# Kernel tuning notes

Hardware: AMD Instinct MI355X
Metric: run time of the kernel (lower is better)

The kernel has to match this reference:

```python
import jax, jax.numpy as jnp
import numpy as np

N, D, H = 262144, 512, 128


def _mlp(x, W1, b1, W2, b2):
    # Linear -> ReLU -> Linear
    return jax.nn.relu(x @ W1 + b1) @ W2 + b2


def setup_inputs() -> dict:
    key = jax.random.key(0)
    ks = jax.random.split(key, 8)
    features = jax.random.normal(ks[0], (N, D), dtype=jnp.float32)
    # last column is the routing flag: 0 -> transform expert, nonzero -> actor expert
    flags = jax.random.randint(ks[1], (N,), 0, 2).astype(jnp.float32)
    features = features.at[:, -1].set(flags)
    s = 0.02
    return {
        "features": features,
        "Wt1": jax.random.normal(ks[2], (D, H), dtype=jnp.float32) * s,
        "bt1": jnp.zeros((H,), dtype=jnp.float32),
        "Wt2": jax.random.normal(ks[3], (H, H), dtype=jnp.float32) * s,
        "bt2": jnp.zeros((H,), dtype=jnp.float32),
        "Wa1": jax.random.normal(ks[4], (D, H), dtype=jnp.float32) * s,
        "ba1": jnp.zeros((H,), dtype=jnp.float32),
        "Wa2": jax.random.normal(ks[5], (H, H), dtype=jnp.float32) * s,
        "ba2": jnp.zeros((H,), dtype=jnp.float32),
        "Wv1": jax.random.normal(ks[6], (D, H), dtype=jnp.float32) * s,
        "bv1": jnp.zeros((H,), dtype=jnp.float32),
        "Wv2": jax.random.normal(ks[7], (H, H), dtype=jnp.float32) * s,
        "bv2": jnp.zeros((H,), dtype=jnp.float32),
    }


def reference(features, Wt1, bt1, Wt2, bt2, Wa1, ba1, Wa2, ba2, Wv1, bv1, Wv2, bv2):
    # forward_actor: per-row dispatch on flag = features[:, -1]
    # flag == 0 -> policy_transform_net, else -> policy_actor_net.
    # Equivalent vectorized form: compute both experts, select per row.
    flag_is_zero = (features[:, -1] == 0)[:, None]  # [N, 1]
    trans_out = _mlp(features, Wt1, bt1, Wt2, bt2)   # [N, H]
    actor_out = _mlp(features, Wa1, ba1, Wa2, ba2)   # [N, H]
    latent_pi = jnp.where(flag_is_zero, trans_out, actor_out)
    # forward_critic: Linear-ReLU-Linear-ReLU
    latent_vf = jax.nn.relu(_mlp(features, Wv1, bv1, Wv2, bv2))
    return latent_pi, latent_vf
```

## Files before the change

### kernel.cpp

```cpp
#include <hip/hip_runtime.h>

#define NTOK 262144L
#define DIN 512
#define HID 128

typedef __attribute__((ext_vector_type(4))) float f32x4;
typedef __attribute__((ext_vector_type(8))) short bf16x8;

static __device__ __forceinline__ unsigned short f2bf(float f) {
  unsigned int u = __builtin_bit_cast(unsigned int, f);
  u += 0x7fffu + ((u >> 16) & 1u);
  return (unsigned short)(u >> 16);
}

__global__ void pack_w(const float* __restrict__ Wt1, const float* __restrict__ Wa1,
                       const float* __restrict__ Wv1, const float* __restrict__ Wt2,
                       const float* __restrict__ Wa2, const float* __restrict__ Wv2,
                       unsigned short* __restrict__ pk) {
  int idx = blockIdx.x * 256 + threadIdx.x;
  if (idx >= 245760) return;
  float v;
  if (idx < 196608) {
    int j = idx & 7, l = (idx >> 3) & 63, ct = (idx >> 9) & 7, kt = (idx >> 12) & 15, e = idx >> 16;
    const float* W = (e == 0) ? Wt1 : (e == 1) ? Wa1 : Wv1;
    v = W[(kt * 32 + ((l >> 4) * 8) + j) * HID + ct * 16 + (l & 15)];
  } else {
    int i2 = idx - 196608;
    int j = i2 & 7, l = (i2 >> 3) & 63, ct = (i2 >> 9) & 7, kt = (i2 >> 12) & 3, e = i2 >> 14;
    const float* W = (e == 0) ? Wt2 : (e == 1) ? Wa2 : Wv2;
    v = W[(kt * 32 + ((l >> 4) * 8) + j) * HID + ct * 16 + (l & 15)];
  }
  pk[idx] = f2bf(v);
}

template <int MODE>
static __device__ __forceinline__ void expert_pass(
    const unsigned short* Xs, unsigned short* Hs,
    const unsigned short* __restrict__ W1f, const unsigned short* __restrict__ W2f,
    const float* __restrict__ b1, const float* __restrict__ b2,
    float* __restrict__ ob, long brow,
    int lane, int l15, int g, int w, const unsigned short* flg,
    f32x4 keep[4][2])
{
  const int cb = 2 * w;

  f32x4 acc[4][2];
  #pragma unroll
  for (int c = 0; c < 2; ++c) {
    float bv = b1[(cb + c) * 16 + l15];
    #pragma unroll
    for (int rt = 0; rt < 4; ++rt) {
      acc[rt][c][0] = bv; acc[rt][c][1] = bv; acc[rt][c][2] = bv; acc[rt][c][3] = bv;
    }
  }
  #pragma unroll
  for (int kt = 0; kt < 16; ++kt) {
    bf16x8 bA = *(const bf16x8*)(W1f + ((kt * 8 + cb) << 9) + (lane << 3));
    bf16x8 bB = *(const bf16x8*)(W1f + ((kt * 8 + cb + 1) << 9) + (lane << 3));
    #pragma unroll
    for (int rt = 0; rt < 4; ++rt) {
      int row = rt * 16 + l15;
      bf16x8 a = *(const bf16x8*)((const char*)Xs +
                   ((row * 1024 + kt * 64 + g * 16) ^ ((row & 7) << 4)));
      acc[rt][0] = __builtin_amdgcn_mfma_f32_16x16x32_bf16(a, bA, acc[rt][0], 0, 0, 0);
      acc[rt][1] = __builtin_amdgcn_mfma_f32_16x16x32_bf16(a, bB, acc[rt][1], 0, 0, 0);
    }
  }

  __syncthreads();

  #pragma unroll
  for (int rt = 0; rt < 4; ++rt)
    #pragma unroll
    for (int c = 0; c < 2; ++c)
      #pragma unroll
      for (int r = 0; r < 4; ++r) {
        int row = rt * 16 + 4 * g + r;
        int col = (cb + c) * 16 + l15;
        int ha = (row * 256 + col * 2) ^ ((row & 7) << 4);
        *(unsigned short*)((char*)Hs + ha) = f2bf(fmaxf(acc[rt][c][r], 0.f));
      }
  __syncthreads();

  f32x4 a2[4][2];
  #pragma unroll
  for (int c = 0; c < 2; ++c) {
    float bv = b2[(cb + c) * 16 + l15];
    #pragma unroll
    for (int rt = 0; rt < 4; ++rt) {
      a2[rt][c][0] = bv; a2[rt][c][1] = bv; a2[rt][c][2] = bv; a2[rt][c][3] = bv;
    }
  }
  #pragma unroll
  for (int kt = 0; kt < 4; ++kt) {
    bf16x8 bA = *(const bf16x8*)(W2f + ((kt * 8 + cb) << 9) + (lane << 3));
    bf16x8 bB = *(const bf16x8*)(W2f + ((kt * 8 + cb + 1) << 9) + (lane << 3));
    #pragma unroll
    for (int rt = 0; rt < 4; ++rt) {
      int row = rt * 16 + l15;
      bf16x8 a = *(const bf16x8*)((const char*)Hs +
                   ((row * 256 + kt * 64 + g * 16) ^ ((row & 7) << 4)));
      a2[rt][0] = __builtin_amdgcn_mfma_f32_16x16x32_bf16(a, bA, a2[rt][0], 0, 0, 0);
      a2[rt][1] = __builtin_amdgcn_mfma_f32_16x16x32_bf16(a, bB, a2[rt][1], 0, 0, 0);
    }
  }

  #pragma unroll
  for (int rt = 0; rt < 4; ++rt)
    #pragma unroll
    for (int c = 0; c < 2; ++c)
      #pragma unroll
      for (int r = 0; r < 4; ++r) {
        float v = a2[rt][c][r];
        if (MODE == 0) {
          keep[rt][c][r] = v;
        } else {
          long row = brow + rt * 16 + 4 * g + r;
          long col = (cb + c) * 16 + l15;
          if (MODE == 1) {
            float sel = (flg[rt * 4 + r] == 0) ? keep[rt][c][r] : v;
            ob[row * 128 + col] = sel;
          } else {
            ob[row * 128 + col] = fmaxf(v, 0.f);
          }
        }
      }
}

__global__ __launch_bounds__(256, 2) void mlp3(
    const float* __restrict__ X, const unsigned short* __restrict__ pk,
    const float* __restrict__ bt1, const float* __restrict__ bt2,
    const float* __restrict__ ba1, const float* __restrict__ ba2,
    const float* __restrict__ bv1, const float* __restrict__ bv2,
    float* __restrict__ out) {
  __shared__ unsigned short Xs[64 * 512];
  __shared__ unsigned short Hs[64 * 128];
  const int t = threadIdx.x;
  const long brow = (long)blockIdx.x * 64;

  const float4* Xv = (const float4*)(X + brow * DIN);
  #pragma unroll
  for (int i = 0; i < 32; ++i) {
    int f = t + i * 256;
    int row = f >> 7, c4 = f & 127;
    float4 v = Xv[f];
    unsigned long long p = (unsigned long long)f2bf(v.x)
                         | ((unsigned long long)f2bf(v.y) << 16)
                         | ((unsigned long long)f2bf(v.z) << 32)
                         | ((unsigned long long)f2bf(v.w) << 48);
    int addr = (row * 1024 + c4 * 8) ^ ((row & 7) << 4);
    *(unsigned long long*)((char*)Xs + addr) = p;
  }
  __syncthreads();

  const int lane = t & 63;
  const int w = t >> 6;
  const int l15 = lane & 15;
  const int g = lane >> 4;

  unsigned short flg[16];
  #pragma unroll
  for (int rt = 0; rt < 4; ++rt)
    #pragma unroll
    for (int r = 0; r < 4; ++r) {
      int row = rt * 16 + 4 * g + r;
      flg[rt * 4 + r] = *(const unsigned short*)((const char*)Xs +
                          ((row * 1024 + 1022) ^ ((row & 7) << 4)));
    }

  f32x4 keep[4][2];
  expert_pass<0>(Xs, Hs, pk,           pk + 196608, bt1, bt2, out, brow, lane, l15, g, w, flg, keep);
  expert_pass<1>(Xs, Hs, pk + 65536,   pk + 212992, ba1, ba2, out, brow, lane, l15, g, w, flg, keep);
  expert_pass<2>(Xs, Hs, pk + 131072,  pk + 229376, bv1, bv2, out + NTOK * 128, brow, lane, l15, g, w, flg, keep);
}

extern "C" void kernel_launch(void* const* d_in, const int* in_sizes, int n_in,
                              void* d_out, int out_size, void* d_ws, size_t ws_size,
                              hipStream_t stream) {
  const float* X   = (const float*)d_in[0];
  const float* Wt1 = (const float*)d_in[1];
  const float* bt1 = (const float*)d_in[2];
  const float* Wt2 = (const float*)d_in[3];
  const float* bt2 = (const float*)d_in[4];
  const float* Wa1 = (const float*)d_in[5];
  const float* ba1 = (const float*)d_in[6];
  const float* Wa2 = (const float*)d_in[7];
  const float* ba2 = (const float*)d_in[8];
  const float* Wv1 = (const float*)d_in[9];
  const float* bv1 = (const float*)d_in[10];
  const float* Wv2 = (const float*)d_in[11];
  const float* bv2 = (const float*)d_in[12];
  unsigned short* pk = (unsigned short*)d_ws;

  pack_w<<<960, 256, 0, stream>>>(Wt1, Wa1, Wv1, Wt2, Wa2, Wv2, pk);
  mlp3<<<4096, 256, 0, stream>>>(X, pk, bt1, bt2, ba1, ba2, bv1, bv2, (float*)d_out);
}
```

Baseline: 280.8 us.

## Stream X in double-buffered K chunks and fuse three experts' first layer

New measurement: 271.7 us. 3.3% less time.

```diff
diff --git a/kernel.cpp b/kernel.cpp
--- a/kernel.cpp
+++ b/kernel.cpp
@@ -1,8 +1,6 @@
 #include <hip/hip_runtime.h>
 
 #define NTOK 262144L
-#define DIN 512
-#define HID 128
 
 typedef __attribute__((ext_vector_type(4))) float f32x4;
 typedef __attribute__((ext_vector_type(8))) short bf16x8;
@@ -23,155 +21,180 @@
   if (idx < 196608) {
     int j = idx & 7, l = (idx >> 3) & 63, ct = (idx >> 9) & 7, kt = (idx >> 12) & 15, e = idx >> 16;
     const float* W = (e == 0) ? Wt1 : (e == 1) ? Wa1 : Wv1;
-    v = W[(kt * 32 + ((l >> 4) * 8) + j) * HID + ct * 16 + (l & 15)];
+    v = W[(kt * 32 + ((l >> 4) * 8) + j) * 128 + ct * 16 + (l & 15)];
   } else {
     int i2 = idx - 196608;
     int j = i2 & 7, l = (i2 >> 3) & 63, ct = (i2 >> 9) & 7, kt = (i2 >> 12) & 3, e = i2 >> 14;
     const float* W = (e == 0) ? Wt2 : (e == 1) ? Wa2 : Wv2;
-    v = W[(kt * 32 + ((l >> 4) * 8) + j) * HID + ct * 16 + (l & 15)];
+    v = W[(kt * 32 + ((l >> 4) * 8) + j) * 128 + ct * 16 + (l & 15)];
   }
   pk[idx] = f2bf(v);
 }
 
-template <int MODE>
-static __device__ __forceinline__ void expert_pass(
-    const unsigned short* Xs, unsigned short* Hs,
-    const unsigned short* __restrict__ W1f, const unsigned short* __restrict__ W2f,
-    const float* __restrict__ b1, const float* __restrict__ b2,
-    float* __restrict__ ob, long brow,
-    int lane, int l15, int g, int w, const unsigned short* flg,
-    f32x4 keep[4][2])
-{
-  const int cb = 2 * w;
-
-  f32x4 acc[4][2];
-  #pragma unroll
-  for (int c = 0; c < 2; ++c) {
-    float bv = b1[(cb + c) * 16 + l15];
-    #pragma unroll
-    for (int rt = 0; rt < 4; ++rt) {
-      acc[rt][c][0] = bv; acc[rt][c][1] = bv; acc[rt][c][2] = bv; acc[rt][c][3] = bv;
-    }
-  }
-  #pragma unroll
-  for (int kt = 0; kt < 16; ++kt) {
-    bf16x8 bA = *(const bf16x8*)(W1f + ((kt * 8 + cb) << 9) + (lane << 3));
-    bf16x8 bB = *(const bf16x8*)(W1f + ((kt * 8 + cb + 1) << 9) + (lane << 3));
-    #pragma unroll
-    for (int rt = 0; rt < 4; ++rt) {
-      int row = rt * 16 + l15;
-      bf16x8 a = *(const bf16x8*)((const char*)Xs +
-                   ((row * 1024 + kt * 64 + g * 16) ^ ((row & 7) << 4)));
-      acc[rt][0] = __builtin_amdgcn_mfma_f32_16x16x32_bf16(a, bA, acc[rt][0], 0, 0, 0);
-      acc[rt][1] = __builtin_amdgcn_mfma_f32_16x16x32_bf16(a, bB, acc[rt][1], 0, 0, 0);
-    }
-  }
-
-  __syncthreads();
-
-  #pragma unroll
-  for (int rt = 0; rt < 4; ++rt)
-    #pragma unroll
-    for (int c = 0; c < 2; ++c)
-      #pragma unroll
-      for (int r = 0; r < 4; ++r) {
-        int row = rt * 16 + 4 * g + r;
-        int col = (cb + c) * 16 + l15;
-        int ha = (row * 256 + col * 2) ^ ((row & 7) << 4);
-        *(unsigned short*)((char*)Hs + ha) = f2bf(fmaxf(acc[rt][c][r], 0.f));
-      }
-  __syncthreads();
-
-  f32x4 a2[4][2];
-  #pragma unroll
-  for (int c = 0; c < 2; ++c) {
-    float bv = b2[(cb + c) * 16 + l15];
-    #pragma unroll
-    for (int rt = 0; rt < 4; ++rt) {
-      a2[rt][c][0] = bv; a2[rt][c][1] = bv; a2[rt][c][2] = bv; a2[rt][c][3] = bv;
-    }
-  }
-  #pragma unroll
-  for (int kt = 0; kt < 4; ++kt) {
-    bf16x8 bA = *(const bf16x8*)(W2f + ((kt * 8 + cb) << 9) + (lane << 3));
-    bf16x8 bB = *(const bf16x8*)(W2f + ((kt * 8 + cb + 1) << 9) + (lane << 3));
-    #pragma unroll
-    for (int rt = 0; rt < 4; ++rt) {
-      int row = rt * 16 + l15;
-      bf16x8 a = *(const bf16x8*)((const char*)Hs +
-                   ((row * 256 + kt * 64 + g * 16) ^ ((row & 7) << 4)));
-      a2[rt][0] = __builtin_amdgcn_mfma_f32_16x16x32_bf16(a, bA, a2[rt][0], 0, 0, 0);
-      a2[rt][1] = __builtin_amdgcn_mfma_f32_16x16x32_bf16(a, bB, a2[rt][1], 0, 0, 0);
-    }
-  }
-
-  #pragma unroll
-  for (int rt = 0; rt < 4; ++rt)
-    #pragma unroll
-    for (int c = 0; c < 2; ++c)
-      #pragma unroll
-      for (int r = 0; r < 4; ++r) {
-        float v = a2[rt][c][r];
-        if (MODE == 0) {
-          keep[rt][c][r] = v;
-        } else {
-          long row = brow + rt * 16 + 4 * g + r;
-          long col = (cb + c) * 16 + l15;
-          if (MODE == 1) {
-            float sel = (flg[rt * 4 + r] == 0) ? keep[rt][c][r] : v;
-            ob[row * 128 + col] = sel;
-          } else {
-            ob[row * 128 + col] = fmaxf(v, 0.f);
-          }
-        }
-      }
-}
-
-__global__ __launch_bounds__(256, 2) void mlp3(
+
+__global__ __launch_bounds__(512, 4) void mlp3(
     const float* __restrict__ X, const unsigned short* __restrict__ pk,
     const float* __restrict__ bt1, const float* __restrict__ bt2,
     const float* __restrict__ ba1, const float* __restrict__ ba2,
     const float* __restrict__ bv1, const float* __restrict__ bv2,
     float* __restrict__ out) {
-  __shared__ unsigned short Xs[64 * 512];
-  __shared__ unsigned short Hs[64 * 128];
+  __shared__ unsigned short Xs[2 * 64 * 128];
+  __shared__ unsigned short Hs[3 * 64 * 128];
   const int t = threadIdx.x;
   const long brow = (long)blockIdx.x * 64;
-
-  const float4* Xv = (const float4*)(X + brow * DIN);
-  #pragma unroll
-  for (int i = 0; i < 32; ++i) {
-    int f = t + i * 256;
-    int row = f >> 7, c4 = f & 127;
-    float4 v = Xv[f];
-    unsigned long long p = (unsigned long long)f2bf(v.x)
-                         | ((unsigned long long)f2bf(v.y) << 16)
-                         | ((unsigned long long)f2bf(v.z) << 32)
-                         | ((unsigned long long)f2bf(v.w) << 48);
-    int addr = (row * 1024 + c4 * 8) ^ ((row & 7) << 4);
-    *(unsigned long long*)((char*)Xs + addr) = p;
-  }
-  __syncthreads();
-
   const int lane = t & 63;
   const int w = t >> 6;
   const int l15 = lane & 15;
   const int g = lane >> 4;
 
-  unsigned short flg[16];
+  const float4* __restrict__ Xv = (const float4*)(X + brow * 512);
+
+  f32x4 at[4], aa[4], av[4];
+  {
+    float b0 = bt1[w * 16 + l15], b1v = ba1[w * 16 + l15], b2v = bv1[w * 16 + l15];
+    #pragma unroll
+    for (int rt = 0; rt < 4; ++rt) {
+      at[rt] = (f32x4){b0, b0, b0, b0};
+      aa[rt] = (f32x4){b1v, b1v, b1v, b1v};
+      av[rt] = (f32x4){b2v, b2v, b2v, b2v};
+    }
+  }
+
+  {
+    float4 ld[4];
+    #pragma unroll
+    for (int i = 0; i < 4; ++i) {
+      int f = t + 512 * i;
+      ld[i] = Xv[(f >> 5) * 128 + (f & 31)];
+    }
+    #pragma unroll
+    for (int i = 0; i < 4; ++i) {
+      int f = t + 512 * i;
+      int row = f >> 5, c4 = f & 31;
+      unsigned long long p = (unsigned long long)f2bf(ld[i].x)
+                           | ((unsigned long long)f2bf(ld[i].y) << 16)
+                           | ((unsigned long long)f2bf(ld[i].z) << 32)
+                           | ((unsigned long long)f2bf(ld[i].w) << 48);
+      int addr = (row * 256 + c4 * 8) ^ ((row & 7) << 4);
+      *(unsigned long long*)((char*)Xs + addr) = p;
+    }
+  }
+  __syncthreads();
+
+  unsigned fmask = 0;
+
+  #pragma unroll
+  for (int kc = 0; kc < 4; ++kc) {
+    float4 nx[4];
+    if (kc < 3) {
+      #pragma unroll
+      for (int i = 0; i < 4; ++i) {
+        int f = t + 512 * i;
+        nx[i] = Xv[(f >> 5) * 128 + (kc + 1) * 32 + (f & 31)];
+      }
+    }
+    const char* xb = (const char*)Xs + (kc & 1) * 16384;
+    #pragma unroll
+    for (int ktl = 0; ktl < 4; ++ktl) {
+      int kt = kc * 4 + ktl;
+      int wo = ((kt * 8 + w) << 9) + (lane << 3);
+      bf16x8 wt = *(const bf16x8*)(pk + wo);
+      bf16x8 wa = *(const bf16x8*)(pk + 65536 + wo);
+      bf16x8 wv = *(const bf16x8*)(pk + 131072 + wo);
+      #pragma unroll
+      for (int rt = 0; rt < 4; ++rt) {
+        int row = rt * 16 + l15;
+        bf16x8 a = *(const bf16x8*)(xb + ((row * 256 + ktl * 64 + g * 16) ^ ((row & 7) << 4)));
+        at[rt] = __builtin_amdgcn_mfma_f32_16x16x32_bf16(a, wt, at[rt], 0, 0, 0);
+        aa[rt] = __builtin_amdgcn_mfma_f32_16x16x32_bf16(a, wa, aa[rt], 0, 0, 0);
+        av[rt] = __builtin_amdgcn_mfma_f32_16x16x32_bf16(a, wv, av[rt], 0, 0, 0);
+      }
+    }
+    if (kc == 3) {
+      #pragma unroll
+      for (int rt = 0; rt < 4; ++rt)
+        #pragma unroll
+        for (int r = 0; r < 4; ++r) {
+          int row = rt * 16 + 4 * g + r;
+          unsigned short fv = *(const unsigned short*)((const char*)Xs + 16384 +
+                               ((row * 256 + 254) ^ ((row & 7) << 4)));
+          if (fv != 0) fmask |= 1u << (rt * 4 + r);
+        }
+    }
+    if (kc < 3) {
+      #pragma unroll
+      for (int i = 0; i < 4; ++i) {
+        int f = t + 512 * i;
+        int row = f >> 5, c4 = f & 31;
+        unsigned long long p = (unsigned long long)f2bf(nx[i].x)
+                             | ((unsigned long long)f2bf(nx[i].y) << 16)
+                             | ((unsigned long long)f2bf(nx[i].z) << 32)
+                             | ((unsigned long long)f2bf(nx[i].w) << 48);
+        int addr = ((kc + 1) & 1) * 16384 + ((row * 256 + c4 * 8) ^ ((row & 7) << 4));
+        *(unsigned long long*)((char*)Xs + addr) = p;
+      }
+      __syncthreads();
+    }
+  }
+
   #pragma unroll
   for (int rt = 0; rt < 4; ++rt)
     #pragma unroll
     for (int r = 0; r < 4; ++r) {
       int row = rt * 16 + 4 * g + r;
-      flg[rt * 4 + r] = *(const unsigned short*)((const char*)Xs +
-                          ((row * 1024 + 1022) ^ ((row & 7) << 4)));
-    }
-
-  f32x4 keep[4][2];
-  expert_pass<0>(Xs, Hs, pk,           pk + 196608, bt1, bt2, out, brow, lane, l15, g, w, flg, keep);
-  expert_pass<1>(Xs, Hs, pk + 65536,   pk + 212992, ba1, ba2, out, brow, lane, l15, g, w, flg, keep);
-  expert_pass<2>(Xs, Hs, pk + 131072,  pk + 229376, bv1, bv2, out + NTOK * 128, brow, lane, l15, g, w, flg, keep);
+      int col = w * 16 + l15;
+      int ha = (row * 256 + col * 2) ^ ((row & 7) << 4) ^ ((row & 8) << 2);
+      *(unsigned short*)((char*)Hs + ha)         = f2bf(fmaxf(at[rt][r], 0.f));
+      *(unsigned short*)((char*)Hs + 16384 + ha) = f2bf(fmaxf(aa[rt][r], 0.f));
+      *(unsigned short*)((char*)Hs + 32768 + ha) = f2bf(fmaxf(av[rt][r], 0.f));
+    }
+  __syncthreads();
+
+  auto layer2 = [&](int e, const float* __restrict__ b2, f32x4 a2[4]) {
+    float bv = b2[w * 16 + l15];
+    #pragma unroll
+    for (int rt = 0; rt < 4; ++rt) a2[rt] = (f32x4){bv, bv, bv, bv};
+    const unsigned short* W2f = pk + 196608 + e * 16384;
+    const char* hb = (const char*)Hs + e * 16384;
+    #pragma unroll
+    for (int kt = 0; kt < 4; ++kt) {
+      bf16x8 wb = *(const bf16x8*)(W2f + ((kt * 8 + w) << 9) + (lane << 3));
+      #pragma unroll
+      for (int rt = 0; rt < 4; ++rt) {
+        int row = rt * 16 + l15;
+        bf16x8 a = *(const bf16x8*)(hb + ((row * 256 + kt * 64 + g * 16)
+                      ^ ((row & 7) << 4) ^ ((row & 8) << 2)));
+        a2[rt] = __builtin_amdgcn_mfma_f32_16x16x32_bf16(a, wb, a2[rt], 0, 0, 0);
+      }
+    }
+  };
+
+  f32x4 keep[4], a2[4];
+  layer2(0, bt2, keep);
+  layer2(1, ba2, a2);
+  {
+    const int col = w * 16 + l15;
+    #pragma unroll
+    for (int rt = 0; rt < 4; ++rt)
+      #pragma unroll
+      for (int r = 0; r < 4; ++r) {
+        long row = brow + rt * 16 + 4 * g + r;
+        float sel = ((fmask >> (rt * 4 + r)) & 1u) ? a2[rt][r] : keep[rt][r];
+        out[row * 128 + col] = sel;
+      }
+  }
+  layer2(2, bv2, a2);
+  {
+    const int col = w * 16 + l15;
+    float* __restrict__ ov = out + NTOK * 128;
+    #pragma unroll
+    for (int rt = 0; rt < 4; ++rt)
+      #pragma unroll
+      for (int r = 0; r < 4; ++r) {
+        long row = brow + rt * 16 + 4 * g + r;
+        ov[row * 128 + col] = fmaxf(a2[rt][r], 0.f);
+      }
+  }
 }
 
 extern "C" void kernel_launch(void* const* d_in, const int* in_sizes, int n_in,
@@ -193,5 +216,5 @@
   unsigned short* pk = (unsigned short*)d_ws;
 
   pack_w<<<960, 256, 0, stream>>>(Wt1, Wa1, Wv1, Wt2, Wa2, Wv2, pk);
-  mlp3<<<4096, 256, 0, stream>>>(X, pk, bt1, bt2, ba1, ba2, bv1, bv2, (float*)d_out);
-}
+  mlp3<<<4096, 512, 0, stream>>>(X, pk, bt1, bt2, ba1, ba2, bv1, bv2, (float*)d_out);
+}
```

## Restructure MLP kernel to per-wave 16-row tiles with swapped MFMA operands

Applied to the files above, without the earlier changes.

New measurement: 501.8 us. +78.7%, slower.

```diff
diff --git a/kernel.cpp b/kernel.cpp
--- a/kernel.cpp
+++ b/kernel.cpp
@@ -1,8 +1,6 @@
 #include <hip/hip_runtime.h>
 
 #define NTOK 262144L
-#define DIN 512
-#define HID 128
 
 typedef __attribute__((ext_vector_type(4))) float f32x4;
 typedef __attribute__((ext_vector_type(8))) short bf16x8;
@@ -12,6 +10,14 @@
   u += 0x7fffu + ((u >> 16) & 1u);
   return (unsigned short)(u >> 16);
 }
+
+static __device__ __forceinline__ unsigned cvtpk(float lo, float hi) {
+  unsigned r;
+  asm("v_cvt_pk_bf16_f32 %0, %1, %2" : "=v"(r) : "v"(lo), "v"(hi));
+  return r;
+}
+
+union U8 { unsigned u[4]; bf16x8 v; };
 
 __global__ void pack_w(const float* __restrict__ Wt1, const float* __restrict__ Wa1,
                        const float* __restrict__ Wv1, const float* __restrict__ Wt2,
@@ -23,155 +29,141 @@
   if (idx < 196608) {
     int j = idx & 7, l = (idx >> 3) & 63, ct = (idx >> 9) & 7, kt = (idx >> 12) & 15, e = idx >> 16;
     const float* W = (e == 0) ? Wt1 : (e == 1) ? Wa1 : Wv1;
-    v = W[(kt * 32 + ((l >> 4) * 8) + j) * HID + ct * 16 + (l & 15)];
+    v = W[(kt * 32 + ((l >> 4) * 8) + j) * 128 + ct * 16 + (l & 15)];
   } else {
     int i2 = idx - 196608;
     int j = i2 & 7, l = (i2 >> 3) & 63, ct = (i2 >> 9) & 7, kt = (i2 >> 12) & 3, e = i2 >> 14;
     const float* W = (e == 0) ? Wt2 : (e == 1) ? Wa2 : Wv2;
-    v = W[(kt * 32 + ((l >> 4) * 8) + j) * HID + ct * 16 + (l & 15)];
+    v = W[(kt * 32 + ((l >> 4) * 8) + j) * 128 + ct * 16 + (l & 15)];
   }
   pk[idx] = f2bf(v);
 }
 
-template <int MODE>
-static __device__ __forceinline__ void expert_pass(
-    const unsigned short* Xs, unsigned short* Hs,
-    const unsigned short* __restrict__ W1f, const unsigned short* __restrict__ W2f,
-    const float* __restrict__ b1, const float* __restrict__ b2,
-    float* __restrict__ ob, long brow,
-    int lane, int l15, int g, int w, const unsigned short* flg,
-    f32x4 keep[4][2])
-{
-  const int cb = 2 * w;
-
-  f32x4 acc[4][2];
-  #pragma unroll
-  for (int c = 0; c < 2; ++c) {
-    float bv = b1[(cb + c) * 16 + l15];
-    #pragma unroll
-    for (int rt = 0; rt < 4; ++rt) {
-      acc[rt][c][0] = bv; acc[rt][c][1] = bv; acc[rt][c][2] = bv; acc[rt][c][3] = bv;
-    }
-  }
-  #pragma unroll
-  for (int kt = 0; kt < 16; ++kt) {
-    bf16x8 bA = *(const bf16x8*)(W1f + ((kt * 8 + cb) << 9) + (lane << 3));
-    bf16x8 bB = *(const bf16x8*)(W1f + ((kt * 8 + cb + 1) << 9) + (lane << 3));
-    #pragma unroll
-    for (int rt = 0; rt < 4; ++rt) {
-      int row = rt * 16 + l15;
-      bf16x8 a = *(const bf16x8*)((const char*)Xs +
-                   ((row * 1024 + kt * 64 + g * 16) ^ ((row & 7) << 4)));
-      acc[rt][0] = __builtin_amdgcn_mfma_f32_16x16x32_bf16(a, bA, acc[rt][0], 0, 0, 0);
-      acc[rt][1] = __builtin_amdgcn_mfma_f32_16x16x32_bf16(a, bB, acc[rt][1], 0, 0, 0);
-    }
-  }
-
-  __syncthreads();
-
-  #pragma unroll
-  for (int rt = 0; rt < 4; ++rt)
-    #pragma unroll
-    for (int c = 0; c < 2; ++c)
-      #pragma unroll
-      for (int r = 0; r < 4; ++r) {
-        int row = rt * 16 + 4 * g + r;
-        int col = (cb + c) * 16 + l15;
-        int ha = (row * 256 + col * 2) ^ ((row & 7) << 4);
-        *(unsigned short*)((char*)Hs + ha) = f2bf(fmaxf(acc[rt][c][r], 0.f));
-      }
-  __syncthreads();
-
-  f32x4 a2[4][2];
-  #pragma unroll
-  for (int c = 0; c < 2; ++c) {
-    float bv = b2[(cb + c) * 16 + l15];
-    #pragma unroll
-    for (int rt = 0; rt < 4; ++rt) {
-      a2[rt][c][0] = bv; a2[rt][c][1] = bv; a2[rt][c][2] = bv; a2[rt][c][3] = bv;
-    }
-  }
-  #pragma unroll
-  for (int kt = 0; kt < 4; ++kt) {
-    bf16x8 bA = *(const bf16x8*)(W2f + ((kt * 8 + cb) << 9) + (lane << 3));
-    bf16x8 bB = *(const bf16x8*)(W2f + ((kt * 8 + cb + 1) << 9) + (lane << 3));
-    #pragma unroll
-    for (int rt = 0; rt < 4; ++rt) {
-      int row = rt * 16 + l15;
-      bf16x8 a = *(const bf16x8*)((const char*)Hs +
-                   ((row * 256 + kt * 64 + g * 16) ^ ((row & 7) << 4)));
-      a2[rt][0] = __builtin_amdgcn_mfma_f32_16x16x32_bf16(a, bA, a2[rt][0], 0, 0, 0);
-      a2[rt][1] = __builtin_amdgcn_mfma_f32_16x16x32_bf16(a, bB, a2[rt][1], 0, 0, 0);
-    }
-  }
-
-  #pragma unroll
-  for (int rt = 0; rt < 4; ++rt)
-    #pragma unroll
-    for (int c = 0; c < 2; ++c)
-      #pragma unroll
-      for (int r = 0; r < 4; ++r) {
-        float v = a2[rt][c][r];
-        if (MODE == 0) {
-          keep[rt][c][r] = v;
-        } else {
-          long row = brow + rt * 16 + 4 * g + r;
-          long col = (cb + c) * 16 + l15;
-          if (MODE == 1) {
-            float sel = (flg[rt * 4 + r] == 0) ? keep[rt][c][r] : v;
-            ob[row * 128 + col] = sel;
-          } else {
-            ob[row * 128 + col] = fmaxf(v, 0.f);
-          }
-        }
-      }
-}
-
-__global__ __launch_bounds__(256, 2) void mlp3(
+__global__ __launch_bounds__(256, 3) void mlp3(
     const float* __restrict__ X, const unsigned short* __restrict__ pk,
     const float* __restrict__ bt1, const float* __restrict__ bt2,
     const float* __restrict__ ba1, const float* __restrict__ ba2,
     const float* __restrict__ bv1, const float* __restrict__ bv2,
     float* __restrict__ out) {
-  __shared__ unsigned short Xs[64 * 512];
-  __shared__ unsigned short Hs[64 * 128];
+  __shared__ char Hs[4][3 * 4096];
   const int t = threadIdx.x;
-  const long brow = (long)blockIdx.x * 64;
-
-  const float4* Xv = (const float4*)(X + brow * DIN);
-  #pragma unroll
-  for (int i = 0; i < 32; ++i) {
-    int f = t + i * 256;
-    int row = f >> 7, c4 = f & 127;
-    float4 v = Xv[f];
-    unsigned long long p = (unsigned long long)f2bf(v.x)
-                         | ((unsigned long long)f2bf(v.y) << 16)
-                         | ((unsigned long long)f2bf(v.z) << 32)
-                         | ((unsigned long long)f2bf(v.w) << 48);
-    int addr = (row * 1024 + c4 * 8) ^ ((row & 7) << 4);
-    *(unsigned long long*)((char*)Xs + addr) = p;
-  }
-  __syncthreads();
-
   const int lane = t & 63;
   const int w = t >> 6;
   const int l15 = lane & 15;
   const int g = lane >> 4;
+  const long myrow = (long)blockIdx.x * 64 + w * 16 + l15;
+  const float* __restrict__ Xr = X + myrow * 512;
+  const int hxor = (l15 & 7) << 4;
+  char* const hw = Hs[w];
 
-  unsigned short flg[16];
+  const float flag = Xr[511];
+
+  f32x4 acc0[8], acc1[8], acc2[8];
   #pragma unroll
-  for (int rt = 0; rt < 4; ++rt)
+  for (int ct = 0; ct < 8; ++ct) {
+    acc0[ct] = *(const f32x4*)(bt1 + ct * 16 + 4 * g);
+    acc1[ct] = *(const f32x4*)(ba1 + ct * 16 + 4 * g);
+    acc2[ct] = *(const f32x4*)(bv1 + ct * 16 + 4 * g);
+  }
+
+  f32x4 xa = *(const f32x4*)(Xr + g * 8);
+  f32x4 xb = *(const f32x4*)(Xr + g * 8 + 4);
+
+  #pragma unroll 1
+  for (int kt = 0; kt < 16; ++kt) {
+    U8 u;
+    u.u[0] = cvtpk(xa[0], xa[1]);
+    u.u[1] = cvtpk(xa[2], xa[3]);
+    u.u[2] = cvtpk(xb[0], xb[1]);
+    u.u[3] = cvtpk(xb[2], xb[3]);
+    if (kt < 15) {
+      xa = *(const f32x4*)(Xr + (kt + 1) * 32 + g * 8);
+      xb = *(const f32x4*)(Xr + (kt + 1) * 32 + g * 8 + 4);
+    }
+    const unsigned short* __restrict__ pb = pk + ((kt * 8) << 9) + (lane << 3);
     #pragma unroll
-    for (int r = 0; r < 4; ++r) {
-      int row = rt * 16 + 4 * g + r;
-      flg[rt * 4 + r] = *(const unsigned short*)((const char*)Xs +
-                          ((row * 1024 + 1022) ^ ((row & 7) << 4)));
+    for (int ct = 0; ct < 8; ++ct) {
+      bf16x8 ft = *(const bf16x8*)(pb + (ct << 9));
+      bf16x8 fa = *(const bf16x8*)(pb + 65536 + (ct << 9));
+      bf16x8 fv = *(const bf16x8*)(pb + 131072 + (ct << 9));
+      acc0[ct] = __builtin_amdgcn_mfma_f32_16x16x32_bf16(ft, u.v, acc0[ct], 0, 0, 0);
+      acc1[ct] = __builtin_amdgcn_mfma_f32_16x16x32_bf16(fa, u.v, acc1[ct], 0, 0, 0);
+      acc2[ct] = __builtin_amdgcn_mfma_f32_16x16x32_bf16(fv, u.v, acc2[ct], 0, 0, 0);
     }
+  }
 
-  f32x4 keep[4][2];
-  expert_pass<0>(Xs, Hs, pk,           pk + 196608, bt1, bt2, out, brow, lane, l15, g, w, flg, keep);
-  expert_pass<1>(Xs, Hs, pk + 65536,   pk + 212992, ba1, ba2, out, brow, lane, l15, g, w, flg, keep);
-  expert_pass<2>(Xs, Hs, pk + 131072,  pk + 229376, bv1, bv2, out + NTOK * 128, brow, lane, l15, g, w, flg, keep);
+  const int hbase = l15 * 256;
+  #pragma unroll
+  for (int ct = 0; ct < 8; ++ct) {
+    int off = hbase + ((32 * ct + 8 * g) ^ hxor);
+    unsigned long long p0 =
+        (unsigned long long)cvtpk(fmaxf(acc0[ct][0], 0.f), fmaxf(acc0[ct][1], 0.f)) |
+        ((unsigned long long)cvtpk(fmaxf(acc0[ct][2], 0.f), fmaxf(acc0[ct][3], 0.f)) << 32);
+    unsigned long long p1 =
+        (unsigned long long)cvtpk(fmaxf(acc1[ct][0], 0.f), fmaxf(acc1[ct][1], 0.f)) |
+        ((unsigned long long)cvtpk(fmaxf(acc1[ct][2], 0.f), fmaxf(acc1[ct][3], 0.f)) << 32);
+    unsigned long long p2 =
+        (unsigned long long)cvtpk(fmaxf(acc2[ct][0], 0.f), fmaxf(acc2[ct][1], 0.f)) |
+        ((unsigned long long)cvtpk(fmaxf(acc2[ct][2], 0.f), fmaxf(acc2[ct][3], 0.f)) << 32);
+    *(unsigned long long*)(hw + off) = p0;
+    *(unsigned long long*)(hw + 4096 + off) = p1;
+    *(unsigned long long*)(hw + 8192 + off) = p2;
+  }
+
+  const unsigned short* __restrict__ W2 = pk + 196608;
+  f32x4 r0[8], r1[8];
+  #pragma unroll
+  for (int ct = 0; ct < 8; ++ct) {
+    r0[ct] = *(const f32x4*)(bt2 + ct * 16 + 4 * g);
+    r1[ct] = *(const f32x4*)(ba2 + ct * 16 + 4 * g);
+  }
+  #pragma unroll
+  for (int s = 0; s < 4; ++s) {
+    bf16x8 h0 = *(const bf16x8*)(hw + hbase + ((64 * s + 16 * g) ^ hxor));
+    bf16x8 h1 = *(const bf16x8*)(hw + 4096 + hbase + ((64 * s + 16 * g) ^ hxor));
+    const unsigned short* __restrict__ qb = W2 + ((s * 8) << 9) + (lane << 3);
+    #pragma unroll
+    for (int ct = 0; ct < 8; ++ct) {
+      r0[ct] = __builtin_amdgcn_mfma_f32_16x16x32_bf16(
+                   *(const bf16x8*)(qb + (ct << 9)), h0, r0[ct], 0, 0, 0);
+      r1[ct] = __builtin_amdgcn_mfma_f32_16x16x32_bf16(
+                   *(const bf16x8*)(qb + 16384 + (ct << 9)), h1, r1[ct], 0, 0, 0);
+    }
+  }
+
+  {
+    const bool sel = (flag != 0.f);
+    float* __restrict__ op = out + myrow * 128;
+    #pragma unroll
+    for (int ct = 0; ct < 8; ++ct) {
+      f32x4 r = sel ? r1[ct] : r0[ct];
+      *(f32x4*)(op + ct * 16 + 4 * g) = r;
+    }
+  }
+
+  f32x4 rv[8];
+  #pragma unroll
+  for (int ct = 0; ct < 8; ++ct)
+    rv[ct] = *(const f32x4*)(bv2 + ct * 16 + 4 * g);
+  #pragma unroll
+  for (int s = 0; s < 4; ++s) {
+    bf16x8 h2 = *(const bf16x8*)(hw + 8192 + hbase + ((64 * s + 16 * g) ^ hxor));
+    const unsigned short* __restrict__ qb = W2 + 32768 + ((s * 8) << 9) + (lane << 3);
+    #pragma unroll
+    for (int ct = 0; ct < 8; ++ct)
+      rv[ct] = __builtin_amdgcn_mfma_f32_16x16x32_bf16(
+                   *(const bf16x8*)(qb + (ct << 9)), h2, rv[ct], 0, 0, 0);
+  }
+  {
+    float* __restrict__ ovp = out + NTOK * 128 + myrow * 128;
+    #pragma unroll
+    for (int ct = 0; ct < 8; ++ct) {
+      f32x4 r = rv[ct];
+      r[0] = fmaxf(r[0], 0.f); r[1] = fmaxf(r[1], 0.f);
+      r[2] = fmaxf(r[2], 0.f); r[3] = fmaxf(r[3], 0.f);
+      *(f32x4*)(ovp + ct * 16 + 4 * g) = r;
+    }
+  }
 }
 
 extern "C" void kernel_launch(void* const* d_in, const int* in_sizes, int n_in,
```
